# Kernel optimization log

Measured on AMD Instinct MI355X. Metric: run time of the kernel, lower is better.

Reference implementation:

```python
import jax, jax.numpy as jnp
import numpy as np

HEAD_SIZE = 16  # matches init_kwargs head_size


def _rope_angles(seq_len, half_dim, base=10000.0):
    # standard RoPE frequencies, matches typical precompute_pos_cis
    freqs = 1.0 / (base ** (np.arange(0, half_dim, dtype=np.float32) / half_dim))
    t = np.arange(seq_len, dtype=np.float32)
    ang = np.outer(t, freqs)  # (S, half_dim)
    return jnp.asarray(np.cos(ang)), jnp.asarray(np.sin(ang))


def setup_inputs() -> dict:
    key = jax.random.key(0)
    ks = jax.random.split(key, 10)
    B, S, D = 2, 2048, 1024
    hd = D // HEAD_SIZE
    pos_cos, pos_sin = _rope_angles(S, hd // 2)
    w = lambda k: jax.random.normal(k, (D, D), jnp.float32) * 0.02
    b = lambda k: jax.random.normal(k, (D,), jnp.float32) * 0.02
    return {
        "x": jax.random.normal(ks[0], (B, S, D), jnp.float32),
        "pos_cos": pos_cos,
        "pos_sin": pos_sin,
        "wq_w": w(ks[1]), "wq_b": b(ks[2]),
        "wk_w": w(ks[3]), "wk_b": b(ks[4]),
        "wv_w": w(ks[5]), "wv_b": b(ks[6]),
        "wo_w": w(ks[7]), "wo_b": b(ks[8]),
    }


def _apply_rope(t, cos, sin):
    # t: (B, S, H, hd); cos/sin: (S, hd//2) -> broadcast (1, S, 1, hd//2)
    B, S, H, hd = t.shape
    tr = t.reshape(B, S, H, hd // 2, 2)
    a, b = tr[..., 0], tr[..., 1]
    c = cos[None, :, None, :]
    s = sin[None, :, None, :]
    # complex multiply (a + ib) * (c + is)
    out_r = a * c - b * s
    out_i = a * s + b * c
    return jnp.stack([out_r, out_i], axis=-1).reshape(B, S, H, hd)


def reference(x, pos_cos, pos_sin, wq_w, wq_b, wk_w, wk_b, wv_w, wv_b, wo_w, wo_b):
    B, S, D = x.shape
    H = HEAD_SIZE
    hd = D // H
    q = (x @ wq_w.T + wq_b).reshape(B, S, H, hd)
    k = (x @ wk_w.T + wk_b).reshape(B, S, H, hd)
    v = (x @ wv_w.T + wv_b).reshape(B, S, H, hd)
    q = _apply_rope(q, pos_cos, pos_sin)
    k = _apply_rope(k, pos_cos, pos_sin)
    scale = 1.0 / jnp.sqrt(jnp.asarray(hd, x.dtype))
    scores = jnp.einsum('bshd,bthd->bhst', q, k) * scale  # (B,H,S,S)
    causal = jnp.tril(jnp.ones((S, S), bool))
    scores = jnp.where(causal[None, None], scores, jnp.asarray(-jnp.inf, scores.dtype))
    probs = jax.nn.softmax(scores, axis=-1)
    out = jnp.einsum('bhst,bthd->bshd', probs, v).reshape(B, S, D)
    return out @ wo_w.T + wo_b
```

## Files before the change

### kernel.cpp

```cpp
#include <hip/hip_runtime.h>
#include <stdint.h>
#include <stddef.h>


typedef __bf16 bf16x8 __attribute__((ext_vector_type(8)));
typedef float  f32x4  __attribute__((ext_vector_type(4)));

__device__ __forceinline__ unsigned short f2b(float f) {
  union { float f; uint32_t u; } v; v.f = f;
  uint32_t u = v.u;
  return (unsigned short)((u + 0x7FFFu + ((u >> 16) & 1u)) >> 16);
}

__device__ __forceinline__ void async16(const void* g, void* l) {
  __builtin_amdgcn_global_load_lds(
      (const __attribute__((address_space(1))) void*)g,
      (__attribute__((address_space(3))) void*)l, 16, 0, 0);
}

__global__ void cast_kernel(const float* __restrict__ in,
                            unsigned short* __restrict__ out, int n4) {
  int i = blockIdx.x * blockDim.x + threadIdx.x;
  if (i >= n4) return;
  float4 v = ((const float4*)in)[i];
  ushort4 o;
  o.x = f2b(v.x); o.y = f2b(v.y); o.z = f2b(v.z); o.w = f2b(v.w);
  ((ushort4*)out)[i] = o;
}

__global__ void cast_w_kernel(const float* __restrict__ wq, const float* __restrict__ wk,
                              const float* __restrict__ wv, const float* __restrict__ wo,
                              unsigned short* __restrict__ wqkv,
                              unsigned short* __restrict__ wobf) {
  int i = blockIdx.x * blockDim.x + threadIdx.x;
  const int sel = i >> 18, k = i & ((1 << 18) - 1);
  const float* src = (sel == 0) ? wq : (sel == 1) ? wk : (sel == 2) ? wv : wo;
  float4 v = ((const float4*)src)[k];
  ushort4 o;
  o.x = f2b(v.x); o.y = f2b(v.y); o.z = f2b(v.z); o.w = f2b(v.w);
  if (sel < 3) ((ushort4*)wqkv)[(size_t)sel * 262144 + k] = o;
  else         ((ushort4*)wobf)[k] = o;
}

__global__ __launch_bounds__(256) void qkv_gemm_kernel(
    const unsigned short* __restrict__ A,
    const unsigned short* __restrict__ W,
    const float* __restrict__ biasq, const float* __restrict__ biask,
    const float* __restrict__ biasv,
    const float* __restrict__ cp, const float* __restrict__ sp,
    unsigned short* __restrict__ qo,
    unsigned short* __restrict__ ko,
    unsigned short* __restrict__ vo)
{
  __shared__ unsigned short As[128 * 64];
  __shared__ unsigned short Bs[128 * 64];
  const int tid  = threadIdx.x;
  const int w    = tid >> 6, l = tid & 63;
  const int lm   = l & 15,  quad = l >> 4;
  const int nblk = blockIdx.x;
  const int m0   = blockIdx.y * 128;
  const int n0g  = nblk * 128;
  const int wm   = (w >> 1) * 64, wn = (w & 1) * 64;

  const f32x4 fzero = {0.f, 0.f, 0.f, 0.f};
  f32x4 acc[4][4];
#pragma unroll
  for (int i = 0; i < 4; ++i)
#pragma unroll
    for (int j = 0; j < 4; ++j) acc[i][j] = fzero;

  for (int k0 = 0; k0 < 1024; k0 += 64) {
    __syncthreads();
#pragma unroll
    for (int q = 0; q < 4; ++q) {
      const int row = w * 16 + lm + (q & 1) * 64;
      const int kc  = quad + (q >> 1) * 4;
      const size_t ldsb = ((size_t)(w + 4 * (q & 1)) * 128 + 64 * (q >> 1)) * 8;
      async16(A + (size_t)(m0 + row) * 1024 + k0 + kc * 8, As + ldsb);
      async16(W + (size_t)(n0g + row) * 1024 + k0 + kc * 8, Bs + ldsb);
    }
    __syncthreads();
#pragma unroll
    for (int kk = 0; kk < 2; ++kk) {
      bf16x8 af[4], bfc[4];
#pragma unroll
      for (int i = 0; i < 4; ++i)
        af[i] = *(const bf16x8*)(As + (size_t)((((w >> 1) * 4 + i) * 128 + kk * 64 + l)) * 8);
#pragma unroll
      for (int j = 0; j < 4; ++j)
        bfc[j] = *(const bf16x8*)(Bs + (size_t)((((w & 1) * 4 + j) * 128 + kk * 64 + l)) * 8);
#pragma unroll
      for (int i = 0; i < 4; ++i)
#pragma unroll
        for (int j = 0; j < 4; ++j)
          acc[i][j] = __builtin_amdgcn_mfma_f32_16x16x32_bf16(af[i], bfc[j], acc[i][j], 0, 0, 0);
    }
  }

  const int which = nblk >> 3;
  const int n0    = (nblk & 7) * 128;
  const float* bias = (which == 0) ? biasq : (which == 1) ? biask : biasv;
#pragma unroll
  for (int i = 0; i < 4; ++i) {
#pragma unroll
    for (int j = 0; j < 4; ++j) {
      const int n = n0 + wn + j * 16 + lm;
      const float bval = bias[n];
      const int h = n >> 6, d = n & 63;
      float vals[4];
#pragma unroll
      for (int r = 0; r < 4; ++r) {
        const int m = m0 + wm + i * 16 + quad * 4 + r;
        const int srow = m & 2047;
        float val = acc[i][j][r] + bval;
        if (which != 2) {
          const float c  = cp[srow * 32 + (d >> 1)];
          const float sn = sp[srow * 32 + (d >> 1)];
          const float part = __shfl_xor(val, 1, 64);
          val = (d & 1) ? (part * sn + val * c) : (val * c - part * sn);
        }
        vals[r] = val;
      }
      const int mbase = m0 + wm + i * 16 + quad * 4;
      const int b = mbase >> 11, s0 = mbase & 2047;
      const int bh = (b << 4) + h;
      if (which == 0) {
#pragma unroll
        for (int r = 0; r < 4; ++r)
          qo[((size_t)bh * 2048 + s0 + r) * 64 + d] = f2b(vals[r]);
      } else if (which == 1) {
#pragma unroll
        for (int r = 0; r < 4; ++r) {
          const int s = s0 + r;
          ko[((size_t)bh * 32 + (s >> 6)) * 4096 +
             (size_t)(((d >> 3) * 64 + (s & 63))) * 8 + (d & 7)] = f2b(vals[r]);
        }
      } else {
        uint32_t w0 = (uint32_t)f2b(vals[0]) | ((uint32_t)f2b(vals[1]) << 16);
        uint32_t w1 = (uint32_t)f2b(vals[2]) | ((uint32_t)f2b(vals[3]) << 16);
        uint2 pk; pk.x = w0; pk.y = w1;
        *(uint2*)(vo + ((size_t)bh * 32 + (s0 >> 6)) * 4096 +
                  (size_t)((((s0 & 63) >> 3) * 64 + d)) * 8 + (s0 & 7)) = pk;
      }
    }
  }
}

__global__ __launch_bounds__(512, 4) void flash_kernel(
    const unsigned short* __restrict__ Q,
    const unsigned short* __restrict__ K,
    const unsigned short* __restrict__ VT,
    unsigned short* __restrict__ O)
{
  constexpr int PSTRIDE = 72;
  __shared__ unsigned short Ps[128 * PSTRIDE];
  const int tid = threadIdx.x;
  const int w = tid >> 6, l = tid & 63, lm = l & 15, quad = l >> 4;
  const int bh = blockIdx.x, qb = 15 - blockIdx.y;
  const int mrow_g = qb * 128 + w * 16 + lm;

  const size_t qbase = ((size_t)bh * 2048 + (size_t)qb * 128) * 64;
  bf16x8 aq[2];
#pragma unroll
  for (int kc = 0; kc < 2; ++kc)
    aq[kc] = *(const bf16x8*)(Q + qbase + (size_t)(w * 16 + lm) * 64 + kc * 32 + quad * 8);

  const f32x4 fzero = {0.f, 0.f, 0.f, 0.f};
  f32x4 Oacc[4];
#pragma unroll
  for (int jo = 0; jo < 4; ++jo) Oacc[jo] = fzero;
  float m_i = -1e30f, l_i = 0.f;

  const int nkv = 2 * qb + 2;
  for (int kt = 0; kt < nkv; ++kt) {
    const size_t tbase = ((size_t)bh * 32 + kt) * 4096;

    f32x4 Sc[4];
#pragma unroll
    for (int tb = 0; tb < 4; ++tb) Sc[tb] = fzero;
#pragma unroll
    for (int kc = 0; kc < 2; ++kc) {
      bf16x8 ak[4];
#pragma unroll
      for (int tb = 0; tb < 4; ++tb)
        ak[tb] = *(const bf16x8*)(K + tbase + (size_t)(((kc * 4 + quad) * 64 + tb * 16 + lm)) * 8);
#pragma unroll
      for (int tb = 0; tb < 4; ++tb)
        Sc[tb] = __builtin_amdgcn_mfma_f32_16x16x32_bf16(ak[tb], aq[kc], Sc[tb], 0, 0, 0);
    }

    const bool needmask = (kt * 64 + 63 > qb * 128 + w * 16);
    const int  mrel = mrow_g - kt * 64;
    float mx = -1e30f;
#pragma unroll
    for (int tb = 0; tb < 4; ++tb) {
#pragma unroll
      for (int r = 0; r < 4; ++r) {
        float s = Sc[tb][r] * 0.125f;
        if (needmask && (tb * 16 + quad * 4 + r > mrel)) s = -1e30f;
        Sc[tb][r] = s;
        mx = fmaxf(mx, s);
      }
    }
    mx = fmaxf(mx, __shfl_xor(mx, 16, 64));
    mx = fmaxf(mx, __shfl_xor(mx, 32, 64));
    const float mnew  = fmaxf(m_i, mx);
    const float alpha = __expf(m_i - mnew);
    m_i = mnew;

    float ps = 0.f;
#pragma unroll
    for (int tb = 0; tb < 4; ++tb) {
      float p0 = __expf(Sc[tb][0] - mnew), p1 = __expf(Sc[tb][1] - mnew);
      float p2 = __expf(Sc[tb][2] - mnew), p3 = __expf(Sc[tb][3] - mnew);
      ps += (p0 + p1) + (p2 + p3);
      uint2 pk;
      pk.x = (uint32_t)f2b(p0) | ((uint32_t)f2b(p1) << 16);
      pk.y = (uint32_t)f2b(p2) | ((uint32_t)f2b(p3) << 16);
      *(uint2*)(Ps + (size_t)(w * 16 + lm) * PSTRIDE + tb * 16 + quad * 4) = pk;
    }
    ps += __shfl_xor(ps, 16, 64);
    ps += __shfl_xor(ps, 32, 64);
    l_i = l_i * alpha + ps;

    float af4[4];
#pragma unroll
    for (int r = 0; r < 4; ++r) af4[r] = __shfl(alpha, quad * 4 + r, 64);
#pragma unroll
    for (int jo = 0; jo < 4; ++jo)
#pragma unroll
      for (int r = 0; r < 4; ++r) Oacc[jo][r] *= af4[r];

#pragma unroll
    for (int kc = 0; kc < 2; ++kc) {
      bf16x8 ap = *(const bf16x8*)(Ps + (size_t)(w * 16 + lm) * PSTRIDE + kc * 32 + quad * 8);
      bf16x8 bv[4];
#pragma unroll
      for (int jo = 0; jo < 4; ++jo)
        bv[jo] = *(const bf16x8*)(VT + tbase + (size_t)(((kc * 4 + quad) * 64 + jo * 16 + lm)) * 8);
#pragma unroll
      for (int jo = 0; jo < 4; ++jo)
        Oacc[jo] = __builtin_amdgcn_mfma_f32_16x16x32_bf16(ap, bv[jo], Oacc[jo], 0, 0, 0);
    }
  }

  float lf[4];
#pragma unroll
  for (int r = 0; r < 4; ++r) lf[r] = 1.0f / __shfl(l_i, quad * 4 + r, 64);
  const int b = bh >> 4, h = bh & 15;
#pragma unroll
  for (int jo = 0; jo < 4; ++jo)
#pragma unroll
    for (int r = 0; r < 4; ++r) {
      const int s   = qb * 128 + w * 16 + quad * 4 + r;
      const int col = h * 64 + jo * 16 + lm;
      O[((size_t)b * 2048 + s) * 1024 + col] = f2b(Oacc[jo][r] * lf[r]);
    }
}

__global__ __launch_bounds__(256) void oproj_gemm_kernel(
    const unsigned short* __restrict__ A,
    const unsigned short* __restrict__ W,
    const float* __restrict__ bias,
    float* __restrict__ out)
{
  __shared__ unsigned short As[64 * 64];
  __shared__ unsigned short Bs[128 * 64];
  const int tid = threadIdx.x;
  const int w = tid >> 6, l = tid & 63;
  const int lm = l & 15, quad = l >> 4;
  const int m0 = blockIdx.y * 64;
  const int n0 = blockIdx.x * 128;

  const f32x4 fzero = {0.f, 0.f, 0.f, 0.f};
  f32x4 acc[4][2];
#pragma unroll
  for (int i = 0; i < 4; ++i)
#pragma unroll
    for (int j = 0; j < 2; ++j) acc[i][j] = fzero;

  for (int k0 = 0; k0 < 1024; k0 += 64) {
    __syncthreads();
#pragma unroll
    for (int q = 0; q < 2; ++q) {
      const int row = w * 16 + lm;
      const int kc  = quad + 4 * q;
      async16(A + (size_t)(m0 + row) * 1024 + k0 + kc * 8,
              As + ((size_t)w * 128 + 64 * q) * 8);
    }
#pragma unroll
    for (int q = 0; q < 4; ++q) {
      const int row = w * 16 + lm + (q & 1) * 64;
      const int kc  = quad + 4 * (q >> 1);
      async16(W + (size_t)(n0 + row) * 1024 + k0 + kc * 8,
              Bs + ((size_t)(w + 4 * (q & 1)) * 128 + 64 * (q >> 1)) * 8);
    }
    __syncthreads();
#pragma unroll
    for (int kk = 0; kk < 2; ++kk) {
      bf16x8 af[4], bfc[2];
#pragma unroll
      for (int i = 0; i < 4; ++i)
        af[i] = *(const bf16x8*)(As + (size_t)((i * 128 + kk * 64 + l)) * 8);
#pragma unroll
      for (int j = 0; j < 2; ++j)
        bfc[j] = *(const bf16x8*)(Bs + (size_t)(((w * 2 + j) * 128 + kk * 64 + l)) * 8);
#pragma unroll
      for (int i = 0; i < 4; ++i)
#pragma unroll
        for (int j = 0; j < 2; ++j)
          acc[i][j] = __builtin_amdgcn_mfma_f32_16x16x32_bf16(af[i], bfc[j], acc[i][j], 0, 0, 0);
    }
  }

#pragma unroll
  for (int i = 0; i < 4; ++i) {
#pragma unroll
    for (int j = 0; j < 2; ++j) {
      const int n = n0 + w * 32 + j * 16 + lm;
      const float bval = bias[n];
#pragma unroll
      for (int r = 0; r < 4; ++r) {
        const int m = m0 + i * 16 + quad * 4 + r;
        out[(size_t)m * 1024 + n] = acc[i][j][r] + bval;
      }
    }
  }
}

extern "C" void kernel_launch(void* const* d_in, const int* in_sizes, int n_in,
                              void* d_out, int out_size, void* d_ws, size_t ws_size,
                              hipStream_t stream) {
  (void)in_sizes; (void)n_in; (void)out_size; (void)ws_size;
  const float* x  = (const float*)d_in[0];
  const float* cp = (const float*)d_in[1];
  const float* sp = (const float*)d_in[2];
  const float* wq = (const float*)d_in[3];
  const float* bq = (const float*)d_in[4];
  const float* wk = (const float*)d_in[5];
  const float* bk = (const float*)d_in[6];
  const float* wv = (const float*)d_in[7];
  const float* bv = (const float*)d_in[8];
  const float* wo = (const float*)d_in[9];
  const float* bo = (const float*)d_in[10];
  float* out = (float*)d_out;

  unsigned short* xbf  = (unsigned short*)d_ws;
  unsigned short* wqkv = xbf  + (size_t)4 * 1024 * 1024;
  unsigned short* wobf = wqkv + (size_t)3 * 1024 * 1024;
  unsigned short* qbf  = wobf + (size_t)1 * 1024 * 1024;
  unsigned short* kbf  = qbf  + (size_t)4 * 1024 * 1024;
  unsigned short* vbf  = kbf  + (size_t)4 * 1024 * 1024;
  unsigned short* obf  = vbf  + (size_t)4 * 1024 * 1024;

  hipLaunchKernelGGL(cast_kernel, dim3(4096), dim3(256), 0, stream, x, xbf, 1048576);
  hipLaunchKernelGGL(cast_w_kernel, dim3(4096), dim3(256), 0, stream,
                     wq, wk, wv, wo, wqkv, wobf);

  hipLaunchKernelGGL(qkv_gemm_kernel, dim3(24, 32), dim3(256), 0, stream,
                     xbf, wqkv, bq, bk, bv, cp, sp, qbf, kbf, vbf);
  hipLaunchKernelGGL(flash_kernel, dim3(32, 16), dim3(512), 0, stream,
                     qbf, kbf, vbf, obf);
  hipLaunchKernelGGL(oproj_gemm_kernel, dim3(8, 64), dim3(256), 0, stream,
                     obf, wobf, bo, out);
}
```

Measured before the change: 240.0 us.

## Give each flash wave two query row-blocks and double-buffer K fragments in registers

The flash kernel now uses 256-thread blocks in which each wave handles 32 query rows as two 16-row halves. K and V fragments loaded from global memory are shared across both halves, halving per-row K/V load traffic. K fragments for the next tile are prefetched into a second register set while the current tile is computed. The cost is higher register pressure, with launch bounds relaxed to (256,2), fewer waves per block, and an unroll-1 loop that processes KV tiles in pairs.

```diff
diff --git a/kernel.cpp b/kernel.cpp
--- a/kernel.cpp
+++ b/kernel.cpp
@@ -146,7 +146,7 @@
   }
 }
 
-__global__ __launch_bounds__(512, 4) void flash_kernel(
+__global__ __launch_bounds__(256, 2) void flash_kernel(
     const unsigned short* __restrict__ Q,
     const unsigned short* __restrict__ K,
     const unsigned short* __restrict__ VT,
@@ -157,105 +157,142 @@
   const int tid = threadIdx.x;
   const int w = tid >> 6, l = tid & 63, lm = l & 15, quad = l >> 4;
   const int bh = blockIdx.x, qb = 15 - blockIdx.y;
-  const int mrow_g = qb * 128 + w * 16 + lm;
-
-  const size_t qbase = ((size_t)bh * 2048 + (size_t)qb * 128) * 64;
-  bf16x8 aq[2];
-#pragma unroll
-  for (int kc = 0; kc < 2; ++kc)
-    aq[kc] = *(const bf16x8*)(Q + qbase + (size_t)(w * 16 + lm) * 64 + kc * 32 + quad * 8);
+  const int wr0 = qb * 128 + w * 32;
+
+  bf16x8 aq[2][2];
+#pragma unroll
+  for (int rh = 0; rh < 2; ++rh)
+#pragma unroll
+    for (int kc = 0; kc < 2; ++kc)
+      aq[rh][kc] = *(const bf16x8*)(Q + ((size_t)bh * 2048 + wr0 + rh * 16 + lm) * 64
+                                    + kc * 32 + quad * 8);
 
   const f32x4 fzero = {0.f, 0.f, 0.f, 0.f};
-  f32x4 Oacc[4];
-#pragma unroll
-  for (int jo = 0; jo < 4; ++jo) Oacc[jo] = fzero;
-  float m_i = -1e30f, l_i = 0.f;
+  f32x4 Oacc[2][4];
+#pragma unroll
+  for (int rh = 0; rh < 2; ++rh)
+#pragma unroll
+    for (int jo = 0; jo < 4; ++jo) Oacc[rh][jo] = fzero;
+  float m_i[2] = {-1e30f, -1e30f}, l_i[2] = {0.f, 0.f};
 
   const int nkv = 2 * qb + 2;
-  for (int kt = 0; kt < nkv; ++kt) {
-    const size_t tbase = ((size_t)bh * 32 + kt) * 4096;
-
-    f32x4 Sc[4];
-#pragma unroll
-    for (int tb = 0; tb < 4; ++tb) Sc[tb] = fzero;
-#pragma unroll
-    for (int kc = 0; kc < 2; ++kc) {
-      bf16x8 ak[4];
-#pragma unroll
-      for (int tb = 0; tb < 4; ++tb)
-        ak[tb] = *(const bf16x8*)(K + tbase + (size_t)(((kc * 4 + quad) * 64 + tb * 16 + lm)) * 8);
-#pragma unroll
-      for (int tb = 0; tb < 4; ++tb)
-        Sc[tb] = __builtin_amdgcn_mfma_f32_16x16x32_bf16(ak[tb], aq[kc], Sc[tb], 0, 0, 0);
-    }
-
-    const bool needmask = (kt * 64 + 63 > qb * 128 + w * 16);
-    const int  mrel = mrow_g - kt * 64;
-    float mx = -1e30f;
-#pragma unroll
-    for (int tb = 0; tb < 4; ++tb) {
+
+#define FLASH_TILE(KT, KF)                                                    \
+  {                                                                           \
+    const size_t tbv_ = ((size_t)bh * 32 + (KT)) * 4096;                      \
+    bf16x8 vf[2][4];                                                          \
+    _Pragma("unroll")                                                         \
+    for (int kc = 0; kc < 2; ++kc)                                            \
+      _Pragma("unroll")                                                       \
+      for (int jo = 0; jo < 4; ++jo)                                          \
+        vf[kc][jo] = *(const bf16x8*)(VT + tbv_ +                             \
+            (size_t)(((kc * 4 + quad) * 64 + jo * 16 + lm)) * 8);             \
+    float alpha2[2];                                                          \
+    _Pragma("unroll")                                                         \
+    for (int rh = 0; rh < 2; ++rh) {                                          \
+      f32x4 Sc[4];                                                            \
+      _Pragma("unroll")                                                       \
+      for (int tb = 0; tb < 4; ++tb) Sc[tb] = fzero;                          \
+      _Pragma("unroll")                                                       \
+      for (int kc = 0; kc < 2; ++kc)                                          \
+        _Pragma("unroll")                                                     \
+        for (int tb = 0; tb < 4; ++tb)                                        \
+          Sc[tb] = __builtin_amdgcn_mfma_f32_16x16x32_bf16(                   \
+              KF[kc][tb], aq[rh][kc], Sc[tb], 0, 0, 0);                       \
+      const int mrow = wr0 + rh * 16 + lm;                                    \
+      const bool needmask = ((KT) * 64 + 63 > wr0 + rh * 16);                 \
+      const int mrel = mrow - (KT) * 64;                                      \
+      float mx = -1e30f;                                                      \
+      _Pragma("unroll")                                                       \
+      for (int tb = 0; tb < 4; ++tb)                                          \
+        _Pragma("unroll")                                                     \
+        for (int r = 0; r < 4; ++r) {                                         \
+          float s = Sc[tb][r] * 0.125f;                                       \
+          if (needmask && (tb * 16 + quad * 4 + r > mrel)) s = -1e30f;        \
+          Sc[tb][r] = s;                                                      \
+          mx = fmaxf(mx, s);                                                  \
+        }                                                                     \
+      mx = fmaxf(mx, __shfl_xor(mx, 16, 64));                                 \
+      mx = fmaxf(mx, __shfl_xor(mx, 32, 64));                                 \
+      const float mnew = fmaxf(m_i[rh], mx);                                  \
+      alpha2[rh] = __expf(m_i[rh] - mnew);                                    \
+      m_i[rh] = mnew;                                                         \
+      float ps = 0.f;                                                         \
+      _Pragma("unroll")                                                       \
+      for (int tb = 0; tb < 4; ++tb) {                                        \
+        float p0 = __expf(Sc[tb][0] - mnew), p1 = __expf(Sc[tb][1] - mnew);   \
+        float p2 = __expf(Sc[tb][2] - mnew), p3 = __expf(Sc[tb][3] - mnew);   \
+        ps += (p0 + p1) + (p2 + p3);                                          \
+        uint2 pk;                                                             \
+        pk.x = (uint32_t)f2b(p0) | ((uint32_t)f2b(p1) << 16);                 \
+        pk.y = (uint32_t)f2b(p2) | ((uint32_t)f2b(p3) << 16);                 \
+        *(uint2*)(Ps + (size_t)(w * 32 + rh * 16 + lm) * PSTRIDE +            \
+                  tb * 16 + quad * 4) = pk;                                   \
+      }                                                                       \
+      ps += __shfl_xor(ps, 16, 64);                                           \
+      ps += __shfl_xor(ps, 32, 64);                                           \
+      l_i[rh] = l_i[rh] * alpha2[rh] + ps;                                    \
+    }                                                                         \
+    _Pragma("unroll")                                                         \
+    for (int rh = 0; rh < 2; ++rh) {                                          \
+      float af4[4];                                                           \
+      _Pragma("unroll")                                                       \
+      for (int r = 0; r < 4; ++r)                                             \
+        af4[r] = __shfl(alpha2[rh], quad * 4 + r, 64);                        \
+      _Pragma("unroll")                                                       \
+      for (int jo = 0; jo < 4; ++jo)                                          \
+        _Pragma("unroll")                                                     \
+        for (int r = 0; r < 4; ++r) Oacc[rh][jo][r] *= af4[r];                \
+      _Pragma("unroll")                                                       \
+      for (int kc = 0; kc < 2; ++kc) {                                        \
+        bf16x8 ap = *(const bf16x8*)(Ps +                                     \
+            (size_t)(w * 32 + rh * 16 + lm) * PSTRIDE + kc * 32 + quad * 8);  \
+        _Pragma("unroll")                                                     \
+        for (int jo = 0; jo < 4; ++jo)                                        \
+          Oacc[rh][jo] = __builtin_amdgcn_mfma_f32_16x16x32_bf16(             \
+              ap, vf[kc][jo], Oacc[rh][jo], 0, 0, 0);                         \
+      }                                                                       \
+    }                                                                         \
+  }
+
+#define LOADK(KF, KT)                                                         \
+  {                                                                           \
+    const size_t tbk_ = ((size_t)bh * 32 + (KT)) * 4096;                      \
+    _Pragma("unroll")                                                         \
+    for (int kc = 0; kc < 2; ++kc)                                            \
+      _Pragma("unroll")                                                       \
+      for (int tb = 0; tb < 4; ++tb)                                          \
+        KF[kc][tb] = *(const bf16x8*)(K + tbk_ +                              \
+            (size_t)(((kc * 4 + quad) * 64 + tb * 16 + lm)) * 8);             \
+  }
+
+  bf16x8 kfA[2][4], kfB[2][4];
+  LOADK(kfA, 0);
+#pragma unroll 1
+  for (int kt = 0; kt < nkv; kt += 2) {
+    LOADK(kfB, kt + 1);
+    FLASH_TILE(kt, kfA);
+    if (kt + 2 < nkv) LOADK(kfA, kt + 2);
+    FLASH_TILE(kt + 1, kfB);
+  }
+#undef FLASH_TILE
+#undef LOADK
+
+  const int b = bh >> 4, h = bh & 15;
+#pragma unroll
+  for (int rh = 0; rh < 2; ++rh) {
+    float lf[4];
+#pragma unroll
+    for (int r = 0; r < 4; ++r) lf[r] = 1.0f / __shfl(l_i[rh], quad * 4 + r, 64);
+#pragma unroll
+    for (int jo = 0; jo < 4; ++jo)
 #pragma unroll
       for (int r = 0; r < 4; ++r) {
-        float s = Sc[tb][r] * 0.125f;
-        if (needmask && (tb * 16 + quad * 4 + r > mrel)) s = -1e30f;
-        Sc[tb][r] = s;
-        mx = fmaxf(mx, s);
+        const int s   = wr0 + rh * 16 + quad * 4 + r;
+        const int col = h * 64 + jo * 16 + lm;
+        O[((size_t)b * 2048 + s) * 1024 + col] = f2b(Oacc[rh][jo][r] * lf[r]);
       }
-    }
-    mx = fmaxf(mx, __shfl_xor(mx, 16, 64));
-    mx = fmaxf(mx, __shfl_xor(mx, 32, 64));
-    const float mnew  = fmaxf(m_i, mx);
-    const float alpha = __expf(m_i - mnew);
-    m_i = mnew;
-
-    float ps = 0.f;
-#pragma unroll
-    for (int tb = 0; tb < 4; ++tb) {
-      float p0 = __expf(Sc[tb][0] - mnew), p1 = __expf(Sc[tb][1] - mnew);
-      float p2 = __expf(Sc[tb][2] - mnew), p3 = __expf(Sc[tb][3] - mnew);
-      ps += (p0 + p1) + (p2 + p3);
-      uint2 pk;
-      pk.x = (uint32_t)f2b(p0) | ((uint32_t)f2b(p1) << 16);
-      pk.y = (uint32_t)f2b(p2) | ((uint32_t)f2b(p3) << 16);
-      *(uint2*)(Ps + (size_t)(w * 16 + lm) * PSTRIDE + tb * 16 + quad * 4) = pk;
-    }
-    ps += __shfl_xor(ps, 16, 64);
-    ps += __shfl_xor(ps, 32, 64);
-    l_i = l_i * alpha + ps;
-
-    float af4[4];
-#pragma unroll
-    for (int r = 0; r < 4; ++r) af4[r] = __shfl(alpha, quad * 4 + r, 64);
-#pragma unroll
-    for (int jo = 0; jo < 4; ++jo)
-#pragma unroll
-      for (int r = 0; r < 4; ++r) Oacc[jo][r] *= af4[r];
-
-#pragma unroll
-    for (int kc = 0; kc < 2; ++kc) {
-      bf16x8 ap = *(const bf16x8*)(Ps + (size_t)(w * 16 + lm) * PSTRIDE + kc * 32 + quad * 8);
-      bf16x8 bv[4];
-#pragma unroll
-      for (int jo = 0; jo < 4; ++jo)
-        bv[jo] = *(const bf16x8*)(VT + tbase + (size_t)(((kc * 4 + quad) * 64 + jo * 16 + lm)) * 8);
-#pragma unroll
-      for (int jo = 0; jo < 4; ++jo)
-        Oacc[jo] = __builtin_amdgcn_mfma_f32_16x16x32_bf16(ap, bv[jo], Oacc[jo], 0, 0, 0);
-    }
-  }
-
-  float lf[4];
-#pragma unroll
-  for (int r = 0; r < 4; ++r) lf[r] = 1.0f / __shfl(l_i, quad * 4 + r, 64);
-  const int b = bh >> 4, h = bh & 15;
-#pragma unroll
-  for (int jo = 0; jo < 4; ++jo)
-#pragma unroll
-    for (int r = 0; r < 4; ++r) {
-      const int s   = qb * 128 + w * 16 + quad * 4 + r;
-      const int col = h * 64 + jo * 16 + lm;
-      O[((size_t)b * 2048 + s) * 1024 + col] = f2b(Oacc[jo][r] * lf[r]);
-    }
+  }
 }
 
 __global__ __launch_bounds__(256) void oproj_gemm_kernel(
@@ -359,7 +396,7 @@
 
   hipLaunchKernelGGL(qkv_gemm_kernel, dim3(24, 32), dim3(256), 0, stream,
                      xbf, wqkv, bq, bk, bv, cp, sp, qbf, kbf, vbf);
-  hipLaunchKernelGGL(flash_kernel, dim3(32, 16), dim3(512), 0, stream,
+  hipLaunchKernelGGL(flash_kernel, dim3(32, 16), dim3(256), 0, stream,
                      qbf, kbf, vbf, obf);
   hipLaunchKernelGGL(oproj_gemm_kernel, dim3(8, 64), dim3(256), 0, stream,
                      obf, wobf, bo, out);
```

New measurement: 249.1 us. 3.8% more time.

## Shrink flash query tile to 64 rows, peel diagonal tile, add lazy rescale

Applied to the files above, without the earlier changes.

Query tiles in the flash attention kernel shrink from 128 to 64 rows, with 256-thread blocks on a 32x32 grid. This gives more blocks and a finer causal workload split. The masked diagonal KV tile is peeled out of the main loop so full tiles skip the mask test, and K and V fragments are loaded together at the top of each iteration. It also adds a lazy online-softmax rescale that skips the max update and accumulator scaling while the running max grows by at most 8. That saves exp and multiply work but risks larger intermediate values and more register pressure.

```diff
diff --git a/kernel.cpp b/kernel.cpp
--- a/kernel.cpp
+++ b/kernel.cpp
@@ -146,24 +146,23 @@
   }
 }
 
-__global__ __launch_bounds__(512, 4) void flash_kernel(
+__global__ __launch_bounds__(256, 4) void flash_kernel(
     const unsigned short* __restrict__ Q,
     const unsigned short* __restrict__ K,
     const unsigned short* __restrict__ VT,
     unsigned short* __restrict__ O)
 {
   constexpr int PSTRIDE = 72;
-  __shared__ unsigned short Ps[128 * PSTRIDE];
+  __shared__ unsigned short Ps[64 * PSTRIDE];
   const int tid = threadIdx.x;
   const int w = tid >> 6, l = tid & 63, lm = l & 15, quad = l >> 4;
-  const int bh = blockIdx.x, qb = 15 - blockIdx.y;
-  const int mrow_g = qb * 128 + w * 16 + lm;
-
-  const size_t qbase = ((size_t)bh * 2048 + (size_t)qb * 128) * 64;
+  const int bh = blockIdx.x, qt = 31 - (int)blockIdx.y;
+  const int row0 = qt * 64 + w * 16;
+
   bf16x8 aq[2];
 #pragma unroll
   for (int kc = 0; kc < 2; ++kc)
-    aq[kc] = *(const bf16x8*)(Q + qbase + (size_t)(w * 16 + lm) * 64 + kc * 32 + quad * 8);
+    aq[kc] = *(const bf16x8*)(Q + ((size_t)bh * 2048 + row0 + lm) * 64 + kc * 32 + quad * 8);
 
   const f32x4 fzero = {0.f, 0.f, 0.f, 0.f};
   f32x4 Oacc[4];
@@ -171,37 +170,116 @@
   for (int jo = 0; jo < 4; ++jo) Oacc[jo] = fzero;
   float m_i = -1e30f, l_i = 0.f;
 
-  const int nkv = 2 * qb + 2;
-  for (int kt = 0; kt < nkv; ++kt) {
+  const int nkv = qt + 1;
+
+#pragma unroll 1
+  for (int kt = 0; kt < nkv - 1; ++kt) {
     const size_t tbase = ((size_t)bh * 32 + kt) * 4096;
-
+    bf16x8 kf[2][4], vf[2][4];
+#pragma unroll
+    for (int kc = 0; kc < 2; ++kc)
+#pragma unroll
+      for (int tb = 0; tb < 4; ++tb) {
+        const size_t off = tbase + (size_t)(((kc * 4 + quad) * 64 + tb * 16 + lm)) * 8;
+        kf[kc][tb] = *(const bf16x8*)(K + off);
+        vf[kc][tb] = *(const bf16x8*)(VT + off);
+      }
     f32x4 Sc[4];
 #pragma unroll
     for (int tb = 0; tb < 4; ++tb) Sc[tb] = fzero;
 #pragma unroll
-    for (int kc = 0; kc < 2; ++kc) {
-      bf16x8 ak[4];
+    for (int kc = 0; kc < 2; ++kc)
 #pragma unroll
       for (int tb = 0; tb < 4; ++tb)
-        ak[tb] = *(const bf16x8*)(K + tbase + (size_t)(((kc * 4 + quad) * 64 + tb * 16 + lm)) * 8);
-#pragma unroll
-      for (int tb = 0; tb < 4; ++tb)
-        Sc[tb] = __builtin_amdgcn_mfma_f32_16x16x32_bf16(ak[tb], aq[kc], Sc[tb], 0, 0, 0);
-    }
-
-    const bool needmask = (kt * 64 + 63 > qb * 128 + w * 16);
-    const int  mrel = mrow_g - kt * 64;
+        Sc[tb] = __builtin_amdgcn_mfma_f32_16x16x32_bf16(kf[kc][tb], aq[kc], Sc[tb], 0, 0, 0);
+
     float mx = -1e30f;
 #pragma unroll
-    for (int tb = 0; tb < 4; ++tb) {
+    for (int tb = 0; tb < 4; ++tb)
 #pragma unroll
       for (int r = 0; r < 4; ++r) {
         float s = Sc[tb][r] * 0.125f;
-        if (needmask && (tb * 16 + quad * 4 + r > mrel)) s = -1e30f;
         Sc[tb][r] = s;
         mx = fmaxf(mx, s);
       }
-    }
+    mx = fmaxf(mx, __shfl_xor(mx, 16, 64));
+    mx = fmaxf(mx, __shfl_xor(mx, 32, 64));
+
+    const bool skip = (bool)__all(mx - m_i <= 8.0f);
+    float alpha = 1.f;
+    if (!skip) {
+      const float mnew = fmaxf(m_i, mx);
+      alpha = __expf(m_i - mnew);
+      m_i = mnew;
+    }
+    const float mref = m_i;
+
+    float ps = 0.f;
+#pragma unroll
+    for (int tb = 0; tb < 4; ++tb) {
+      float p0 = __expf(Sc[tb][0] - mref), p1 = __expf(Sc[tb][1] - mref);
+      float p2 = __expf(Sc[tb][2] - mref), p3 = __expf(Sc[tb][3] - mref);
+      ps += (p0 + p1) + (p2 + p3);
+      uint2 pk;
+      pk.x = (uint32_t)f2b(p0) | ((uint32_t)f2b(p1) << 16);
+      pk.y = (uint32_t)f2b(p2) | ((uint32_t)f2b(p3) << 16);
+      *(uint2*)(Ps + (size_t)(w * 16 + lm) * PSTRIDE + tb * 16 + quad * 4) = pk;
+    }
+    ps += __shfl_xor(ps, 16, 64);
+    ps += __shfl_xor(ps, 32, 64);
+    if (skip) {
+      l_i += ps;
+    } else {
+      l_i = l_i * alpha + ps;
+      float af4[4];
+#pragma unroll
+      for (int r = 0; r < 4; ++r) af4[r] = __shfl(alpha, quad * 4 + r, 64);
+#pragma unroll
+      for (int jo = 0; jo < 4; ++jo)
+#pragma unroll
+        for (int r = 0; r < 4; ++r) Oacc[jo][r] *= af4[r];
+    }
+
+#pragma unroll
+    for (int kc = 0; kc < 2; ++kc) {
+      bf16x8 ap = *(const bf16x8*)(Ps + (size_t)(w * 16 + lm) * PSTRIDE + kc * 32 + quad * 8);
+#pragma unroll
+      for (int jo = 0; jo < 4; ++jo)
+        Oacc[jo] = __builtin_amdgcn_mfma_f32_16x16x32_bf16(ap, vf[kc][jo], Oacc[jo], 0, 0, 0);
+    }
+  }
+
+  {
+    const size_t tbase = ((size_t)bh * 32 + qt) * 4096;
+    bf16x8 kf[2][4], vf[2][4];
+#pragma unroll
+    for (int kc = 0; kc < 2; ++kc)
+#pragma unroll
+      for (int tb = 0; tb < 4; ++tb) {
+        const size_t off = tbase + (size_t)(((kc * 4 + quad) * 64 + tb * 16 + lm)) * 8;
+        kf[kc][tb] = *(const bf16x8*)(K + off);
+        vf[kc][tb] = *(const bf16x8*)(VT + off);
+      }
+    f32x4 Sc[4];
+#pragma unroll
+    for (int tb = 0; tb < 4; ++tb) Sc[tb] = fzero;
+#pragma unroll
+    for (int kc = 0; kc < 2; ++kc)
+#pragma unroll
+      for (int tb = 0; tb < 4; ++tb)
+        Sc[tb] = __builtin_amdgcn_mfma_f32_16x16x32_bf16(kf[kc][tb], aq[kc], Sc[tb], 0, 0, 0);
+
+    const int mrel = w * 16 + lm;
+    float mx = -1e30f;
+#pragma unroll
+    for (int tb = 0; tb < 4; ++tb)
+#pragma unroll
+      for (int r = 0; r < 4; ++r) {
+        float s = Sc[tb][r] * 0.125f;
+        if (tb * 16 + quad * 4 + r > mrel) s = -1e30f;
+        Sc[tb][r] = s;
+        mx = fmaxf(mx, s);
+      }
     mx = fmaxf(mx, __shfl_xor(mx, 16, 64));
     mx = fmaxf(mx, __shfl_xor(mx, 32, 64));
     const float mnew  = fmaxf(m_i, mx);
@@ -234,13 +312,9 @@
 #pragma unroll
     for (int kc = 0; kc < 2; ++kc) {
       bf16x8 ap = *(const bf16x8*)(Ps + (size_t)(w * 16 + lm) * PSTRIDE + kc * 32 + quad * 8);
-      bf16x8 bv[4];
 #pragma unroll
       for (int jo = 0; jo < 4; ++jo)
-        bv[jo] = *(const bf16x8*)(VT + tbase + (size_t)(((kc * 4 + quad) * 64 + jo * 16 + lm)) * 8);
-#pragma unroll
-      for (int jo = 0; jo < 4; ++jo)
-        Oacc[jo] = __builtin_amdgcn_mfma_f32_16x16x32_bf16(ap, bv[jo], Oacc[jo], 0, 0, 0);
+        Oacc[jo] = __builtin_amdgcn_mfma_f32_16x16x32_bf16(ap, vf[kc][jo], Oacc[jo], 0, 0, 0);
     }
   }
 
@@ -252,7 +326,7 @@
   for (int jo = 0; jo < 4; ++jo)
 #pragma unroll
     for (int r = 0; r < 4; ++r) {
-      const int s   = qb * 128 + w * 16 + quad * 4 + r;
+      const int s   = row0 + quad * 4 + r;
       const int col = h * 64 + jo * 16 + lm;
       O[((size_t)b * 2048 + s) * 1024 + col] = f2b(Oacc[jo][r] * lf[r]);
     }
@@ -359,7 +433,7 @@
 
   hipLaunchKernelGGL(qkv_gemm_kernel, dim3(24, 32), dim3(256), 0, stream,
                      xbf, wqkv, bq, bk, bv, cp, sp, qbf, kbf, vbf);
-  hipLaunchKernelGGL(flash_kernel, dim3(32, 16), dim3(512), 0, stream,
+  hipLaunchKernelGGL(flash_kernel, dim3(32, 32), dim3(256), 0, stream,
                      qbf, kbf, vbf, obf);
   hipLaunchKernelGGL(oproj_gemm_kernel, dim3(8, 64), dim3(256), 0, stream,
                      obf, wobf, bo, out);
```

Result: faster. 226.7 us (-5.5%).
